# Optimization experiments

Hardware: AMD Instinct MI355X
Metric: run time of the kernel (lower is better)

Reference implementation:

```python
import jax, jax.numpy as jnp
import numpy as np

Np_, Ny, Nu = 5, 8, 4
NZ = Np_ * (Ny + Nu)  # 60


def setup_inputs() -> dict:
    key = jax.random.key(0)
    ks = jax.random.split(key, 6)
    B, T = 8192, 1024
    u = jax.random.normal(ks[0], (B, T, Nu), dtype=jnp.float32)
    z0 = jax.random.normal(ks[1], (B, NZ), dtype=jnp.float32)
    W1 = jax.random.normal(ks[2], (NZ, 128), dtype=jnp.float32) * (1.0 / np.sqrt(NZ))
    b1 = jnp.zeros((128,), dtype=jnp.float32)
    W2 = jax.random.normal(ks[3], (128, 128), dtype=jnp.float32) * (1.0 / np.sqrt(128))
    b2 = jnp.zeros((128,), dtype=jnp.float32)
    W3 = jax.random.normal(ks[4], (128, Ny), dtype=jnp.float32) * (1.0 / np.sqrt(128))
    b3 = jnp.zeros((Ny,), dtype=jnp.float32)
    return {"u": u, "z0": z0, "W1": W1, "b1": b1, "W2": W2, "b2": b2,
            "W3": W3, "b3": b3}


def reference(u, z0, W1, b1, W2, b2, W3, b3):
    # u: [B, T, Nu], z0: [B, Np*(Ny+Nu)] -> y sequence [B, T, Ny]
    def step(z, u_t):
        h = jnp.tanh(z @ W1 + b1)
        h = jnp.tanh(h @ W2 + b2)
        y = h @ W3 + b3                      # [B, Ny]
        ypseq = z[:, : Np_ * Ny]
        upseq = z[:, Np_ * Ny:]
        z_new = jnp.concatenate(
            (ypseq[:, Ny:], y, upseq[:, Nu:], u_t), axis=-1)
        return z_new, y

    u_tbc = jnp.transpose(u, (1, 0, 2))      # [T, B, Nu]
    _, ys = jax.lax.scan(step, z0, u_tbc)    # ys: [T, B, Ny]
    return jnp.transpose(ys, (1, 0, 2))      # [B, T, Ny]
```

## Files before the change

kernel.cpp:

```cpp
#include <hip/hip_runtime.h>

#define T_STEPS 1024
#define NZV 60
#define H 128
#define NY 8
#define NU 4
#define ZSTR 72
#define HSTR 136

typedef __attribute__((ext_vector_type(8))) short bf16x8;
typedef __attribute__((ext_vector_type(4))) short bf16x4;
typedef __attribute__((ext_vector_type(4))) float f32x4;

union U4 { unsigned u[4]; bf16x8 v; };

__device__ __forceinline__ unsigned short f2bf(float x) {
    unsigned u = __float_as_uint(x);
    u += 0x7FFFu + ((u >> 16) & 1u);
    return (unsigned short)(u >> 16);
}

__device__ __forceinline__ unsigned cvt_pk_bf16(float lo, float hi) {
    unsigned r;
    asm("v_cvt_pk_bf16_f32 %0, %1, %2" : "=v"(r) : "v"(lo), "v"(hi));
    return r;
}

__device__ __forceinline__ float tanh_fast(float x) {
    float e = __builtin_amdgcn_exp2f(x * 2.8853900817779268f);
    return fmaf(-2.0f, __builtin_amdgcn_rcpf(e + 1.0f), 1.0f);
}

#define MFMA __builtin_amdgcn_mfma_f32_16x16x32_bf16

__global__ __launch_bounds__(256, 2)
void cstr_scan_kernel(const float* __restrict__ u_g, const float* __restrict__ z0_g,
                      const float* __restrict__ W1, const float* __restrict__ b1,
                      const float* __restrict__ W2, const float* __restrict__ b2,
                      const float* __restrict__ W3, const float* __restrict__ b3,
                      float* __restrict__ out) {
    __shared__ unsigned short zbuf[2][16][ZSTR];
    __shared__ unsigned short h1s[16][HSTR];
    __shared__ unsigned short h2s[2][16][HSTR];
    __shared__ float ybuf[32][16][NY];

    const int tid   = threadIdx.x;
    const int wid   = tid >> 6;
    const int lane  = tid & 63;
    const int b0    = blockIdx.x * 16;
    const int col   = lane & 15;
    const int kg    = lane >> 4;
    const int wrow0 = kg * 4;
    const int urow  = lane >> 2;
    const int uc    = lane & 3;
    const int nbase = wid * 32;
    const int frow  = tid >> 4;
    const int ftoff = tid & 15;

    bf16x8 w1f[2][2], w2f[4][2], w3tf[4];
    float b1v[2], b2v[2];
    f32x4 b3t;
#pragma unroll
    for (int nl = 0; nl < 2; ++nl) {
        b1v[nl] = b1[nbase + nl * 16 + col];
        b2v[nl] = b2[nbase + nl * 16 + col];
    }
#pragma unroll
    for (int r = 0; r < 4; ++r) {
        int m = kg * 4 + r;
        b3t[r] = (m < NY) ? b3[m] : 0.f;
    }
#pragma unroll
    for (int kc = 0; kc < 2; ++kc)
#pragma unroll
        for (int nl = 0; nl < 2; ++nl) {
            bf16x8 v;
#pragma unroll
            for (int j = 0; j < 8; ++j) {
                int k = kc * 32 + kg * 8 + j;
                float w = (k < NZV) ? W1[k * H + nbase + nl * 16 + col] : 0.f;
                v[j] = (short)f2bf(w);
            }
            w1f[kc][nl] = v;
        }
#pragma unroll
    for (int kc = 0; kc < 4; ++kc)
#pragma unroll
        for (int nl = 0; nl < 2; ++nl) {
            bf16x8 v;
#pragma unroll
            for (int j = 0; j < 8; ++j) {
                int k = kc * 32 + kg * 8 + j;
                v[j] = (short)f2bf(W2[k * H + nbase + nl * 16 + col]);
            }
            w2f[kc][nl] = v;
        }
#pragma unroll
    for (int kc = 0; kc < 4; ++kc) {
        bf16x8 v;
#pragma unroll
        for (int j = 0; j < 8; ++j) {
            int k = kc * 32 + kg * 8 + j;
            float w = (col < NY) ? W3[k * NY + col] : 0.f;
            v[j] = (short)f2bf(w);
        }
        w3tf[kc] = v;
    }

    {
        unsigned short* zs = &zbuf[0][0][0];
        for (int i = tid; i < 2 * 16 * ZSTR; i += 256) zs[i] = 0;
        __syncthreads();
        for (int i = tid; i < 16 * NZV; i += 256) {
            int r = i / NZV, c = i - r * NZV;
            zbuf[0][r][c] = f2bf(z0_g[(size_t)(b0 + r) * NZV + c]);
        }
        __syncthreads();
    }

    const float* uptr = u_g + (size_t)(b0 + urow) * (T_STEPS * NU) + uc;
    float ureg = 0.f, ureg_n = 0.f;
    if (wid == 3) ureg = *uptr;

    {
        bf16x8 za0 = *(const bf16x8*)&zbuf[0][col][kg * 8];
        bf16x8 za1 = *(const bf16x8*)&zbuf[0][col][32 + kg * 8];
#pragma unroll
        for (int nl = 0; nl < 2; ++nl) {
            f32x4 c1 = { b1v[nl], b1v[nl], b1v[nl], b1v[nl] };
            c1 = MFMA(za0, w1f[0][nl], c1, 0, 0, 0);
            c1 = MFMA(za1, w1f[1][nl], c1, 0, 0, 0);
            unsigned p01 = cvt_pk_bf16(tanh_fast(c1[0]), tanh_fast(c1[1]));
            unsigned p23 = cvt_pk_bf16(tanh_fast(c1[2]), tanh_fast(c1[3]));
            const int n = nbase + nl * 16 + col;
            h1s[wrow0 + 0][n] = (unsigned short)p01;
            h1s[wrow0 + 1][n] = (unsigned short)(p01 >> 16);
            h1s[wrow0 + 2][n] = (unsigned short)p23;
            h1s[wrow0 + 3][n] = (unsigned short)(p23 >> 16);
        }
        if (wid == 3) {
            bf16x4 m0 = *(const bf16x4*)&zbuf[0][urow][8 + 8 * uc];
            bf16x4 m1 = *(const bf16x4*)&zbuf[0][urow][12 + 8 * uc];
            bf16x4 m2 = *(const bf16x4*)&zbuf[0][urow][44 + 4 * uc];
            *(bf16x4*)&zbuf[1][urow][8 * uc]      = m0;
            *(bf16x4*)&zbuf[1][urow][8 * uc + 4]  = m1;
            *(bf16x4*)&zbuf[1][urow][40 + 4 * uc] = m2;
            zbuf[1][urow][56 + uc] = f2bf(ureg);
            uptr += NU;
            ureg_n = *uptr;
        }
        __syncthreads();
        bf16x8 ha0 = *(const bf16x8*)&h1s[col][0 * 32 + kg * 8];
        bf16x8 ha1 = *(const bf16x8*)&h1s[col][1 * 32 + kg * 8];
        bf16x8 ha2 = *(const bf16x8*)&h1s[col][2 * 32 + kg * 8];
        bf16x8 ha3 = *(const bf16x8*)&h1s[col][3 * 32 + kg * 8];
#pragma unroll
        for (int nl = 0; nl < 2; ++nl) {
            f32x4 a0 = { b2v[nl], b2v[nl], b2v[nl], b2v[nl] };
            f32x4 a1 = { 0.f, 0.f, 0.f, 0.f };
            a0 = MFMA(ha0, w2f[0][nl], a0, 0, 0, 0);
            a1 = MFMA(ha1, w2f[1][nl], a1, 0, 0, 0);
            a0 = MFMA(ha2, w2f[2][nl], a0, 0, 0, 0);
            a1 = MFMA(ha3, w2f[3][nl], a1, 0, 0, 0);
            f32x4 c2 = a0 + a1;
            unsigned p01 = cvt_pk_bf16(tanh_fast(c2[0]), tanh_fast(c2[1]));
            unsigned p23 = cvt_pk_bf16(tanh_fast(c2[2]), tanh_fast(c2[3]));
            const int n = nbase + nl * 16 + col;
            h2s[1][wrow0 + 0][n] = (unsigned short)p01;
            h2s[1][wrow0 + 1][n] = (unsigned short)(p01 >> 16);
            h2s[1][wrow0 + 2][n] = (unsigned short)p23;
            h2s[1][wrow0 + 3][n] = (unsigned short)(p23 >> 16);
        }
        __syncthreads();
        ureg = ureg_n;
    }

    int t = 1;

#define BODY(P)                                                                         \
    {                                                                                   \
        bf16x8 hp0 = *(const bf16x8*)&h2s[P][col][0 * 32 + kg * 8];                     \
        bf16x8 hp1 = *(const bf16x8*)&h2s[P][col][1 * 32 + kg * 8];                     \
        bf16x8 hp2 = *(const bf16x8*)&h2s[P][col][2 * 32 + kg * 8];                     \
        bf16x8 hp3 = *(const bf16x8*)&h2s[P][col][3 * 32 + kg * 8];                     \
        bf16x8 za0  = *(const bf16x8*)&zbuf[P][col][kg * 8];                            \
        bf16x8 za1l = *(const bf16x8*)&zbuf[P][col][32 + kg * 8];                       \
        f32x4 ya = b3t;                                                                 \
        f32x4 yb = { 0.f, 0.f, 0.f, 0.f };                                              \
        ya = MFMA(w3tf[0], hp0, ya, 0, 0, 0);                                           \
        yb = MFMA(w3tf[1], hp1, yb, 0, 0, 0);                                           \
        ya = MFMA(w3tf[2], hp2, ya, 0, 0, 0);                                           \
        yb = MFMA(w3tf[3], hp3, yb, 0, 0, 0);                                           \
        f32x4 yv = ya + yb;               \
        unsigned d0 = cvt_pk_bf16(yv[0], yv[1]);                                        \
        unsigned d1 = cvt_pk_bf16(yv[2], yv[3]);                                        \
        unsigned o0 = (unsigned)__shfl((int)d0, col + 16);                              \
        unsigned o1 = (unsigned)__shfl((int)d1, col + 16);                              \
        U4 zb_; zb_.u[0] = d0; zb_.u[1] = d1; zb_.u[2] = o0; zb_.u[3] = o1;             \
        bf16x8 za1 = (kg == 0) ? zb_.v : za1l;      \
        if (wid == 0 && kg < 2) {                                                       \
            *(f32x4*)&ybuf[(t - 1) & 31][col][kg * 4] = yv;                             \
            unsigned* zp = (unsigned*)&zbuf[P ^ 1][col][24 + kg * 4];                   \
            zp[0] = d0; zp[1] = d1;                  \
        }                                                                               \
        _Pragma("unroll")                                                               \
        for (int nl = 0; nl < 2; ++nl) {                                                \
            f32x4 c1 = { b1v[nl], b1v[nl], b1v[nl], b1v[nl] };                          \
            c1 = MFMA(za0, w1f[0][nl], c1, 0, 0, 0);                                    \
            c1 = MFMA(za1, w1f[1][nl], c1, 0, 0, 0);                                    \
            unsigned p01 = cvt_pk_bf16(tanh_fast(c1[0]), tanh_fast(c1[1]));             \
            unsigned p23 = cvt_pk_bf16(tanh_fast(c1[2]), tanh_fast(c1[3]));             \
            const int n = nbase + nl * 16 + col;                                        \
            h1s[wrow0 + 0][n] = (unsigned short)p01;                                    \
            h1s[wrow0 + 1][n] = (unsigned short)(p01 >> 16);                            \
            h1s[wrow0 + 2][n] = (unsigned short)p23;                                    \
            h1s[wrow0 + 3][n] = (unsigned short)(p23 >> 16);                            \
        }                                                                               \
        if (wid == 3) {     \
            if (uc < 3) {                                                               \
                bf16x4 m0 = *(const bf16x4*)&zbuf[P][urow][8 + 8 * uc];                 \
                bf16x4 m1 = *(const bf16x4*)&zbuf[P][urow][12 + 8 * uc];                \
                *(bf16x4*)&zbuf[P ^ 1][urow][8 * uc]     = m0;                          \
                *(bf16x4*)&zbuf[P ^ 1][urow][8 * uc + 4] = m1;                          \
            }                                                                           \
            bf16x4 m2 = *(const bf16x4*)&zbuf[P][urow][44 + 4 * uc];                    \
            *(bf16x4*)&zbuf[P ^ 1][urow][40 + 4 * uc] = m2;                             \
            zbuf[P ^ 1][urow][56 + uc] = f2bf(ureg);                                    \
            uptr += NU;                                                                 \
            if (t + 1 < T_STEPS) ureg_n = *uptr;                                        \
        }                                                                               \
        __syncthreads();                                                        \
        bf16x8 ha0 = *(const bf16x8*)&h1s[col][0 * 32 + kg * 8];                        \
        bf16x8 ha1 = *(const bf16x8*)&h1s[col][1 * 32 + kg * 8];                        \
        bf16x8 ha2 = *(const bf16x8*)&h1s[col][2 * 32 + kg * 8];                        \
        bf16x8 ha3 = *(const bf16x8*)&h1s[col][3 * 32 + kg * 8];                        \
        _Pragma("unroll")                                                               \
        for (int nl = 0; nl < 2; ++nl) {                                                \
            f32x4 a0 = { b2v[nl], b2v[nl], b2v[nl], b2v[nl] };                          \
            f32x4 a1 = { 0.f, 0.f, 0.f, 0.f };                                          \
            a0 = MFMA(ha0, w2f[0][nl], a0, 0, 0, 0);                                    \
            a1 = MFMA(ha1, w2f[1][nl], a1, 0, 0, 0);                                    \
            a0 = MFMA(ha2, w2f[2][nl], a0, 0, 0, 0);                                    \
            a1 = MFMA(ha3, w2f[3][nl], a1, 0, 0, 0);                                    \
            f32x4 c2 = a0 + a1;                                                         \
            unsigned p01 = cvt_pk_bf16(tanh_fast(c2[0]), tanh_fast(c2[1]));             \
            unsigned p23 = cvt_pk_bf16(tanh_fast(c2[2]), tanh_fast(c2[3]));             \
            const int n = nbase + nl * 16 + col;                                        \
            h2s[P ^ 1][wrow0 + 0][n] = (unsigned short)p01;                             \
            h2s[P ^ 1][wrow0 + 1][n] = (unsigned short)(p01 >> 16);                     \
            h2s[P ^ 1][wrow0 + 2][n] = (unsigned short)p23;                             \
            h2s[P ^ 1][wrow0 + 3][n] = (unsigned short)(p23 >> 16);                     \
        }                                                                               \
        __syncthreads();                                                        \
        ureg = ureg_n;                                                                  \
        ++t;                                                                            \
    }

#pragma unroll 1
    for (int it = 0; it < 511; ++it) {
        if ((t & 15) == 1 && t > 1) {
            const int bt = t - 17;
            const f32x4* yp = (const f32x4*)&ybuf[(bt & 31) + ftoff][frow][0];
            f32x4 v0 = yp[0], v1 = yp[1];
            float* op = out + ((size_t)(b0 + frow) * T_STEPS + bt + ftoff) * NY;
            *(f32x4*)op = v0;
            *(f32x4*)(op + 4) = v1;
        }
        BODY(1)
        BODY(0)
    }
    BODY(1)
#undef BODY

    {
        bf16x8 hp0 = *(const bf16x8*)&h2s[0][col][0 * 32 + kg * 8];
        bf16x8 hp1 = *(const bf16x8*)&h2s[0][col][1 * 32 + kg * 8];
        bf16x8 hp2 = *(const bf16x8*)&h2s[0][col][2 * 32 + kg * 8];
        bf16x8 hp3 = *(const bf16x8*)&h2s[0][col][3 * 32 + kg * 8];
        f32x4 ya = b3t;
        f32x4 yb = { 0.f, 0.f, 0.f, 0.f };
        ya = MFMA(w3tf[0], hp0, ya, 0, 0, 0);
        yb = MFMA(w3tf[1], hp1, yb, 0, 0, 0);
        ya = MFMA(w3tf[2], hp2, ya, 0, 0, 0);
        yb = MFMA(w3tf[3], hp3, yb, 0, 0, 0);
        f32x4 yv = ya + yb;
        if (wid == 0 && kg < 2)
            *(f32x4*)&ybuf[31][col][kg * 4] = yv;
        __syncthreads();
        const f32x4* yp = (const f32x4*)&ybuf[16 + ftoff][frow][0];
        f32x4 v0 = yp[0], v1 = yp[1];
        float* op = out + ((size_t)(b0 + frow) * T_STEPS + 1008 + ftoff) * NY;
        *(f32x4*)op = v0;
        *(f32x4*)(op + 4) = v1;
    }
}

extern "C" void kernel_launch(void* const* d_in, const int* in_sizes, int n_in,
                              void* d_out, int out_size, void* d_ws, size_t ws_size,
                              hipStream_t stream) {
    (void)in_sizes; (void)n_in; (void)d_ws; (void)ws_size; (void)out_size;
    const float* u  = (const float*)d_in[0];
    const float* z0 = (const float*)d_in[1];
    const float* W1 = (const float*)d_in[2];
    const float* b1 = (const float*)d_in[3];
    const float* W2 = (const float*)d_in[4];
    const float* b2 = (const float*)d_in[5];
    const float* W3 = (const float*)d_in[6];
    const float* b3 = (const float*)d_in[7];
    float* out = (float*)d_out;

    dim3 grid(8192 / 16);
    dim3 block(256);
    cstr_scan_kernel<<<grid, block, 0, stream>>>(u, z0, W1, b1, W2, b2, W3, b3, out);
}
```

Measured before the change: 1.111 ms.

## Split layer-3 GEMM across waves with register h2 and async u prefetch

Layer-2 activations now stay in registers instead of going through a shared h2 buffer. Each wave computes a partial layer-3 output with two 16x16x16 MFMAs over its own 32 hidden units, and the partials are reduced through shared memory in the next step. This removes the h2 LDS round trip and the four serial K=32 MFMAs for y from the critical path. The u inputs are now prefetched in 16-step windows into LDS with global_load_lds, replacing per-step scalar global loads. Operand order, bias layout and packed h1 stores also change, and hand-placed s_nop padding around inline-asm MFMAs adds fixed latency.

```diff
diff --git a/kernel.cpp b/kernel.cpp
--- a/kernel.cpp
+++ b/kernel.cpp
@@ -11,8 +11,10 @@
 typedef __attribute__((ext_vector_type(8))) short bf16x8;
 typedef __attribute__((ext_vector_type(4))) short bf16x4;
 typedef __attribute__((ext_vector_type(4))) float f32x4;
+typedef __attribute__((ext_vector_type(2))) unsigned uint2v;
 
 union U4 { unsigned u[4]; bf16x8 v; };
+union U2 { unsigned u[2]; bf16x4 v; };
 
 __device__ __forceinline__ unsigned short f2bf(float x) {
     unsigned u = __float_as_uint(x);
@@ -31,7 +33,18 @@
     return fmaf(-2.0f, __builtin_amdgcn_rcpf(e + 1.0f), 1.0f);
 }
 
-#define MFMA __builtin_amdgcn_mfma_f32_16x16x32_bf16
+#define MFMA32 __builtin_amdgcn_mfma_f32_16x16x32_bf16
+
+__device__ __forceinline__ f32x4 gemm3_pair(bf16x4 a0, bf16x4 b0,
+                                            bf16x4 a1, bf16x4 b1, f32x4 c) {
+    asm("s_nop 1\n\t"
+        "v_mfma_f32_16x16x16_bf16 %0, %1, %2, %0\n\t"
+        "v_mfma_f32_16x16x16_bf16 %0, %3, %4, %0\n\t"
+        "s_nop 7\n\t"
+        "s_nop 7"
+        : "+v"(c) : "v"(a0), "v"(b0), "v"(a1), "v"(b1));
+    return c;
+}
 
 __global__ __launch_bounds__(256, 2)
 void cstr_scan_kernel(const float* __restrict__ u_g, const float* __restrict__ z0_g,
@@ -41,8 +54,9 @@
                       float* __restrict__ out) {
     __shared__ unsigned short zbuf[2][16][ZSTR];
     __shared__ unsigned short h1s[16][HSTR];
-    __shared__ unsigned short h2s[2][16][HSTR];
+    __shared__ f32x4 ypart[4][64];
     __shared__ float ybuf[32][16][NY];
+    __shared__ float ubuf[2][16][16][NU];
 
     const int tid   = threadIdx.x;
     const int wid   = tid >> 6;
@@ -50,21 +64,22 @@
     const int b0    = blockIdx.x * 16;
     const int col   = lane & 15;
     const int kg    = lane >> 4;
-    const int wrow0 = kg * 4;
     const int urow  = lane >> 2;
     const int uc    = lane & 3;
     const int nbase = wid * 32;
     const int frow  = tid >> 4;
     const int ftoff = tid & 15;
 
-    bf16x8 w1f[2][2], w2f[4][2], w3tf[4];
-    float b1v[2], b2v[2];
-    f32x4 b3t;
-#pragma unroll
-    for (int nl = 0; nl < 2; ++nl) {
-        b1v[nl] = b1[nbase + nl * 16 + col];
-        b2v[nl] = b2[nbase + nl * 16 + col];
-    }
+    bf16x8 w1f[2][2], w2f[4][2];
+    bf16x4 w3a0, w3a1;
+    f32x4 b1t[2], b2t[2], b3t;
+#pragma unroll
+    for (int nl = 0; nl < 2; ++nl)
+#pragma unroll
+        for (int r = 0; r < 4; ++r) {
+            b1t[nl][r] = b1[nbase + nl * 16 + kg * 4 + r];
+            b2t[nl][r] = b2[nbase + nl * 16 + kg * 4 + r];
+        }
 #pragma unroll
     for (int r = 0; r < 4; ++r) {
         int m = kg * 4 + r;
@@ -95,16 +110,26 @@
             }
             w2f[kc][nl] = v;
         }
-#pragma unroll
-    for (int kc = 0; kc < 4; ++kc) {
-        bf16x8 v;
-#pragma unroll
-        for (int j = 0; j < 8; ++j) {
-            int k = kc * 32 + kg * 8 + j;
-            float w = (col < NY) ? W3[k * NY + col] : 0.f;
-            v[j] = (short)f2bf(w);
-        }
-        w3tf[kc] = v;
+    {
+        bf16x4 v0, v1;
+#pragma unroll
+        for (int j = 0; j < 4; ++j) {
+            v0[j] = (short)f2bf((col < NY) ? W3[(nbase + 0  + kg * 4 + j) * NY + col] : 0.f);
+            v1[j] = (short)f2bf((col < NY) ? W3[(nbase + 16 + kg * 4 + j) * NY + col] : 0.f);
+        }
+        w3a0 = v0; w3a1 = v1;
+    }
+
+#define LOAD_UWIN(BI, T0)                                                              \
+    if (wid == 1) {                                                                    \
+        const float* usrc = u_g + (size_t)(b0 + (lane & 15)) * (T_STEPS * NU)          \
+                            + (size_t)((T0) + (lane >> 4)) * NU;                       \
+        _Pragma("unroll")                                                              \
+        for (int k_ = 0; k_ < 4; ++k_)                                                 \
+            __builtin_amdgcn_global_load_lds(                                          \
+                (const __attribute__((address_space(1))) unsigned*)(usrc + k_ * 16),   \
+                (__attribute__((address_space(3))) unsigned*)(&ubuf[BI][k_ * 4][0][0]),\
+                16, 0, 0);                                                             \
     }
 
     {
@@ -115,28 +140,24 @@
             int r = i / NZV, c = i - r * NZV;
             zbuf[0][r][c] = f2bf(z0_g[(size_t)(b0 + r) * NZV + c]);
         }
-        __syncthreads();
-    }
-
-    const float* uptr = u_g + (size_t)(b0 + urow) * (T_STEPS * NU) + uc;
-    float ureg = 0.f, ureg_n = 0.f;
-    if (wid == 3) ureg = *uptr;
+        LOAD_UWIN(0, 0)
+        __syncthreads();
+    }
+
+    bf16x8 za0, za1l;
+    int t = 0;
 
     {
-        bf16x8 za0 = *(const bf16x8*)&zbuf[0][col][kg * 8];
-        bf16x8 za1 = *(const bf16x8*)&zbuf[0][col][32 + kg * 8];
+        bf16x8 pza0 = *(const bf16x8*)&zbuf[0][col][kg * 8];
+        bf16x8 pza1 = *(const bf16x8*)&zbuf[0][col][32 + kg * 8];
 #pragma unroll
         for (int nl = 0; nl < 2; ++nl) {
-            f32x4 c1 = { b1v[nl], b1v[nl], b1v[nl], b1v[nl] };
-            c1 = MFMA(za0, w1f[0][nl], c1, 0, 0, 0);
-            c1 = MFMA(za1, w1f[1][nl], c1, 0, 0, 0);
+            f32x4 c1 = b1t[nl];
+            c1 = MFMA32(w1f[0][nl], pza0, c1, 0, 0, 0);
+            c1 = MFMA32(w1f[1][nl], pza1, c1, 0, 0, 0);
             unsigned p01 = cvt_pk_bf16(tanh_fast(c1[0]), tanh_fast(c1[1]));
             unsigned p23 = cvt_pk_bf16(tanh_fast(c1[2]), tanh_fast(c1[3]));
-            const int n = nbase + nl * 16 + col;
-            h1s[wrow0 + 0][n] = (unsigned short)p01;
-            h1s[wrow0 + 1][n] = (unsigned short)(p01 >> 16);
-            h1s[wrow0 + 2][n] = (unsigned short)p23;
-            h1s[wrow0 + 3][n] = (unsigned short)(p23 >> 16);
+            *(uint2v*)&h1s[col][nbase + nl * 16 + kg * 4] = uint2v{p01, p23};
         }
         if (wid == 3) {
             bf16x4 m0 = *(const bf16x4*)&zbuf[0][urow][8 + 8 * uc];
@@ -145,126 +166,114 @@
             *(bf16x4*)&zbuf[1][urow][8 * uc]      = m0;
             *(bf16x4*)&zbuf[1][urow][8 * uc + 4]  = m1;
             *(bf16x4*)&zbuf[1][urow][40 + 4 * uc] = m2;
-            zbuf[1][urow][56 + uc] = f2bf(ureg);
-            uptr += NU;
-            ureg_n = *uptr;
+            zbuf[1][urow][56 + uc] = f2bf(ubuf[0][0][urow][uc]);
         }
         __syncthreads();
         bf16x8 ha0 = *(const bf16x8*)&h1s[col][0 * 32 + kg * 8];
         bf16x8 ha1 = *(const bf16x8*)&h1s[col][1 * 32 + kg * 8];
         bf16x8 ha2 = *(const bf16x8*)&h1s[col][2 * 32 + kg * 8];
         bf16x8 ha3 = *(const bf16x8*)&h1s[col][3 * 32 + kg * 8];
+        za0  = *(const bf16x8*)&zbuf[1][col][kg * 8];
+        za1l = *(const bf16x8*)&zbuf[1][col][32 + kg * 8];
+        bf16x4 pb0, pb1;
 #pragma unroll
         for (int nl = 0; nl < 2; ++nl) {
-            f32x4 a0 = { b2v[nl], b2v[nl], b2v[nl], b2v[nl] };
+            f32x4 a0 = b2t[nl];
             f32x4 a1 = { 0.f, 0.f, 0.f, 0.f };
-            a0 = MFMA(ha0, w2f[0][nl], a0, 0, 0, 0);
-            a1 = MFMA(ha1, w2f[1][nl], a1, 0, 0, 0);
-            a0 = MFMA(ha2, w2f[2][nl], a0, 0, 0, 0);
-            a1 = MFMA(ha3, w2f[3][nl], a1, 0, 0, 0);
+            a0 = MFMA32(w2f[0][nl], ha0, a0, 0, 0, 0);
+            a1 = MFMA32(w2f[1][nl], ha1, a1, 0, 0, 0);
+            a0 = MFMA32(w2f[2][nl], ha2, a0, 0, 0, 0);
+            a1 = MFMA32(w2f[3][nl], ha3, a1, 0, 0, 0);
             f32x4 c2 = a0 + a1;
-            unsigned p01 = cvt_pk_bf16(tanh_fast(c2[0]), tanh_fast(c2[1]));
-            unsigned p23 = cvt_pk_bf16(tanh_fast(c2[2]), tanh_fast(c2[3]));
-            const int n = nbase + nl * 16 + col;
-            h2s[1][wrow0 + 0][n] = (unsigned short)p01;
-            h2s[1][wrow0 + 1][n] = (unsigned short)(p01 >> 16);
-            h2s[1][wrow0 + 2][n] = (unsigned short)p23;
-            h2s[1][wrow0 + 3][n] = (unsigned short)(p23 >> 16);
-        }
-        __syncthreads();
-        ureg = ureg_n;
-    }
-
-    int t = 1;
+            U2 p; p.u[0] = cvt_pk_bf16(tanh_fast(c2[0]), tanh_fast(c2[1]));
+            p.u[1]       = cvt_pk_bf16(tanh_fast(c2[2]), tanh_fast(c2[3]));
+            if (nl == 0) pb0 = p.v; else pb1 = p.v;
+        }
+        f32x4 yp = (wid == 0) ? b3t : f32x4{0.f, 0.f, 0.f, 0.f};
+        yp = gemm3_pair(w3a0, pb0, w3a1, pb1, yp);
+        ypart[wid][lane] = yp;
+        __syncthreads();
+        t = 1;
+    }
 
 #define BODY(P)                                                                         \
     {                                                                                   \
-        bf16x8 hp0 = *(const bf16x8*)&h2s[P][col][0 * 32 + kg * 8];                     \
-        bf16x8 hp1 = *(const bf16x8*)&h2s[P][col][1 * 32 + kg * 8];                     \
-        bf16x8 hp2 = *(const bf16x8*)&h2s[P][col][2 * 32 + kg * 8];                     \
-        bf16x8 hp3 = *(const bf16x8*)&h2s[P][col][3 * 32 + kg * 8];                     \
-        bf16x8 za0  = *(const bf16x8*)&zbuf[P][col][kg * 8];                            \
-        bf16x8 za1l = *(const bf16x8*)&zbuf[P][col][32 + kg * 8];                       \
-        f32x4 ya = b3t;                                                                 \
-        f32x4 yb = { 0.f, 0.f, 0.f, 0.f };                                              \
-        ya = MFMA(w3tf[0], hp0, ya, 0, 0, 0);                                           \
-        yb = MFMA(w3tf[1], hp1, yb, 0, 0, 0);                                           \
-        ya = MFMA(w3tf[2], hp2, ya, 0, 0, 0);                                           \
-        yb = MFMA(w3tf[3], hp3, yb, 0, 0, 0);                                           \
-        f32x4 yv = ya + yb;               \
-        unsigned d0 = cvt_pk_bf16(yv[0], yv[1]);                                        \
-        unsigned d1 = cvt_pk_bf16(yv[2], yv[3]);                                        \
-        unsigned o0 = (unsigned)__shfl((int)d0, col + 16);                              \
-        unsigned o1 = (unsigned)__shfl((int)d1, col + 16);                              \
+                  \
+        f32x4 y_ = ypart[0][lane] + ypart[1][lane] + ypart[2][lane] + ypart[3][lane];   \
+        unsigned d0 = cvt_pk_bf16(y_[0], y_[1]);                                        \
+        unsigned d1 = cvt_pk_bf16(y_[2], y_[3]);                                        \
+        unsigned o0 = (unsigned)__builtin_amdgcn_ds_swizzle((int)d0, 0x401F);           \
+        unsigned o1 = (unsigned)__builtin_amdgcn_ds_swizzle((int)d1, 0x401F);           \
         U4 zb_; zb_.u[0] = d0; zb_.u[1] = d1; zb_.u[2] = o0; zb_.u[3] = o1;             \
         bf16x8 za1 = (kg == 0) ? zb_.v : za1l;      \
-        if (wid == 0 && kg < 2) {                                                       \
-            *(f32x4*)&ybuf[(t - 1) & 31][col][kg * 4] = yv;                             \
-            unsigned* zp = (unsigned*)&zbuf[P ^ 1][col][24 + kg * 4];                   \
-            zp[0] = d0; zp[1] = d1;                  \
+        if (wid == 1 && kg < 2) {                                                       \
+            *(f32x4*)&ybuf[(t - 1) & 31][col][kg * 4] = y_;                             \
+            *(uint2v*)&zbuf[(P) ^ 1][col][24 + kg * 4] = uint2v{d0, d1};                \
         }                                                                               \
         _Pragma("unroll")                                                               \
         for (int nl = 0; nl < 2; ++nl) {                                                \
-            f32x4 c1 = { b1v[nl], b1v[nl], b1v[nl], b1v[nl] };                          \
-            c1 = MFMA(za0, w1f[0][nl], c1, 0, 0, 0);                                    \
-            c1 = MFMA(za1, w1f[1][nl], c1, 0, 0, 0);                                    \
+            f32x4 c1 = b1t[nl];                                                         \
+            c1 = MFMA32(w1f[0][nl], za0, c1, 0, 0, 0);                                  \
+            c1 = MFMA32(w1f[1][nl], za1, c1, 0, 0, 0);                                  \
             unsigned p01 = cvt_pk_bf16(tanh_fast(c1[0]), tanh_fast(c1[1]));             \
             unsigned p23 = cvt_pk_bf16(tanh_fast(c1[2]), tanh_fast(c1[3]));             \
-            const int n = nbase + nl * 16 + col;                                        \
-            h1s[wrow0 + 0][n] = (unsigned short)p01;                                    \
-            h1s[wrow0 + 1][n] = (unsigned short)(p01 >> 16);                            \
-            h1s[wrow0 + 2][n] = (unsigned short)p23;                                    \
-            h1s[wrow0 + 3][n] = (unsigned short)(p23 >> 16);                            \
+            *(uint2v*)&h1s[col][nbase + nl * 16 + kg * 4] = uint2v{p01, p23};           \
         }                                                                               \
-        if (wid == 3) {     \
+        if (wid == 3) {    \
             if (uc < 3) {                                                               \
                 bf16x4 m0 = *(const bf16x4*)&zbuf[P][urow][8 + 8 * uc];                 \
                 bf16x4 m1 = *(const bf16x4*)&zbuf[P][urow][12 + 8 * uc];                \
-                *(bf16x4*)&zbuf[P ^ 1][urow][8 * uc]     = m0;                          \
-                *(bf16x4*)&zbuf[P ^ 1][urow][8 * uc + 4] = m1;                          \
+                *(bf16x4*)&zbuf[(P) ^ 1][urow][8 * uc]     = m0;                        \
+                *(bf16x4*)&zbuf[(P) ^ 1][urow][8 * uc + 4] = m1;                        \
             }                                                                           \
             bf16x4 m2 = *(const bf16x4*)&zbuf[P][urow][44 + 4 * uc];                    \
-            *(bf16x4*)&zbuf[P ^ 1][urow][40 + 4 * uc] = m2;                             \
-            zbuf[P ^ 1][urow][56 + uc] = f2bf(ureg);                                    \
-            uptr += NU;                                                                 \
-            if (t + 1 < T_STEPS) ureg_n = *uptr;                                        \
+            *(bf16x4*)&zbuf[(P) ^ 1][urow][40 + 4 * uc] = m2;                           \
+            zbuf[(P) ^ 1][urow][56 + uc] = f2bf(ubuf[(t >> 4) & 1][t & 15][urow][uc]);  \
         }                                                                               \
-        __syncthreads();                                                        \
+        __syncthreads();                          \
         bf16x8 ha0 = *(const bf16x8*)&h1s[col][0 * 32 + kg * 8];                        \
         bf16x8 ha1 = *(const bf16x8*)&h1s[col][1 * 32 + kg * 8];                        \
         bf16x8 ha2 = *(const bf16x8*)&h1s[col][2 * 32 + kg * 8];                        \
         bf16x8 ha3 = *(const bf16x8*)&h1s[col][3 * 32 + kg * 8];                        \
+        za0  = *(const bf16x8*)&zbuf[(P) ^ 1][col][kg * 8];            \
+        za1l = *(const bf16x8*)&zbuf[(P) ^ 1][col][32 + kg * 8];                        \
+        bf16x4 pb0, pb1;                                                                \
         _Pragma("unroll")                                                               \
         for (int nl = 0; nl < 2; ++nl) {                                                \
-            f32x4 a0 = { b2v[nl], b2v[nl], b2v[nl], b2v[nl] };                          \
+            f32x4 a0 = b2t[nl];                                                         \
             f32x4 a1 = { 0.f, 0.f, 0.f, 0.f };                                          \
-            a0 = MFMA(ha0, w2f[0][nl], a0, 0, 0, 0);                                    \
-            a1 = MFMA(ha1, w2f[1][nl], a1, 0, 0, 0);                                    \
-            a0 = MFMA(ha2, w2f[2][nl], a0, 0, 0, 0);                                    \
-            a1 = MFMA(ha3, w2f[3][nl], a1, 0, 0, 0);                                    \
+            a0 = MFMA32(w2f[0][nl], ha0, a0, 0, 0, 0);                                  \
+            a1 = MFMA32(w2f[1][nl], ha1, a1, 0, 0, 0);                                  \
+            a0 = MFMA32(w2f[2][nl], ha2, a0, 0, 0, 0);                                  \
+            a1 = MFMA32(w2f[3][nl], ha3, a1, 0, 0, 0);                                  \
             f32x4 c2 = a0 + a1;                                                         \
-            unsigned p01 = cvt_pk_bf16(tanh_fast(c2[0]), tanh_fast(c2[1]));             \
-            unsigned p23 = cvt_pk_bf16(tanh_fast(c2[2]), tanh_fast(c2[3]));             \
-            const int n = nbase + nl * 16 + col;                                        \
-            h2s[P ^ 1][wrow0 + 0][n] = (unsigned short)p01;                             \
-            h2s[P ^ 1][wrow0 + 1][n] = (unsigned short)(p01 >> 16);                     \
-            h2s[P ^ 1][wrow0 + 2][n] = (unsigned short)p23;                             \
-            h2s[P ^ 1][wrow0 + 3][n] = (unsigned short)(p23 >> 16);                     \
+            U2 p; p.u[0] = cvt_pk_bf16(tanh_fast(c2[0]), tanh_fast(c2[1]));             \
+            p.u[1]       = cvt_pk_bf16(tanh_fast(c2[2]), tanh_fast(c2[3]));             \
+            if (nl == 0) pb0 = p.v; else pb1 = p.v;                                     \
         }                                                                               \
-        __syncthreads();                                                        \
-        ureg = ureg_n;                                                                  \
+        f32x4 yp = (wid == 0) ? b3t : f32x4{0.f, 0.f, 0.f, 0.f};                        \
+        yp = gemm3_pair(w3a0, pb0, w3a1, pb1, yp);                                      \
+        ypart[wid][lane] = yp;                                                          \
+        __syncthreads();                             \
         ++t;                                                                            \
+    }
+
+#define FLUSH(BT)                                                                       \
+    {                                                                                   \
+        const f32x4* yp_ = (const f32x4*)&ybuf[((BT) & 31) + ftoff][frow][0];           \
+        f32x4 v0 = yp_[0], v1 = yp_[1];                                                 \
+        float* op = out + ((size_t)(b0 + frow) * T_STEPS + (BT) + ftoff) * NY;          \
+        *(f32x4*)op = v0;                                                               \
+        *(f32x4*)(op + 4) = v1;                                                         \
     }
 
 #pragma unroll 1
     for (int it = 0; it < 511; ++it) {
-        if ((t & 15) == 1 && t > 1) {
-            const int bt = t - 17;
-            const f32x4* yp = (const f32x4*)&ybuf[(bt & 31) + ftoff][frow][0];
-            f32x4 v0 = yp[0], v1 = yp[1];
-            float* op = out + ((size_t)(b0 + frow) * T_STEPS + bt + ftoff) * NY;
-            *(f32x4*)op = v0;
-            *(f32x4*)(op + 4) = v1;
+        if ((t & 15) == 1) {
+            if (t > 1)
+                FLUSH(t - 17)
+            if (t + 15 < T_STEPS)
+                LOAD_UWIN((((t + 15) >> 4) & 1), t + 15)
         }
         BODY(1)
         BODY(0)
@@ -273,26 +282,18 @@
 #undef BODY
 
     {
-        bf16x8 hp0 = *(const bf16x8*)&h2s[0][col][0 * 32 + kg * 8];
-        bf16x8 hp1 = *(const bf16x8*)&h2s[0][col][1 * 32 + kg * 8];
-        bf16x8 hp2 = *(const bf16x8*)&h2s[0][col][2 * 32 + kg * 8];
-        bf16x8 hp3 = *(const bf16x8*)&h2s[0][col][3 * 32 + kg * 8];
-        f32x4 ya = b3t;
-        f32x4 yb = { 0.f, 0.f, 0.f, 0.f };
-        ya = MFMA(w3tf[0], hp0, ya, 0, 0, 0);
-        yb = MFMA(w3tf[1], hp1, yb, 0, 0, 0);
-        ya = MFMA(w3tf[2], hp2, ya, 0, 0, 0);
-        yb = MFMA(w3tf[3], hp3, yb, 0, 0, 0);
-        f32x4 yv = ya + yb;
-        if (wid == 0 && kg < 2)
-            *(f32x4*)&ybuf[31][col][kg * 4] = yv;
-        __syncthreads();
-        const f32x4* yp = (const f32x4*)&ybuf[16 + ftoff][frow][0];
-        f32x4 v0 = yp[0], v1 = yp[1];
+        f32x4 y_ = ypart[0][lane] + ypart[1][lane] + ypart[2][lane] + ypart[3][lane];
+        if (wid == 1 && kg < 2)
+            *(f32x4*)&ybuf[31][col][kg * 4] = y_;
+        __syncthreads();
+        const f32x4* yp_ = (const f32x4*)&ybuf[16 + ftoff][frow][0];
+        f32x4 v0 = yp_[0], v1 = yp_[1];
         float* op = out + ((size_t)(b0 + frow) * T_STEPS + 1008 + ftoff) * NY;
         *(f32x4*)op = v0;
         *(f32x4*)(op + 4) = v1;
     }
+#undef FLUSH
+#undef LOAD_UWIN
 }
 
 extern "C" void kernel_launch(void* const* d_in, const int* in_sizes, int n_in,
```

Result: faster. 979.0 us (-11.9%).
